# Performance work log

Measured on AMD Instinct MI355X. Metric: run time of the kernel, lower is better.

## Reference

```python
import jax, jax.numpy as jnp
import numpy as np

NUM_CLASSES = 80
POS_OVERLAP = 0.5
NEG_OVERLAP = 0.4
REG_MEAN = 0.0
REG_STD = 0.2


def setup_inputs() -> dict:
    key = jax.random.key(0)
    k1, k2, k3, k4, k5 = jax.random.split(key, 5)
    B, N, A = 8, 64, 120000
    IMG = 800.0
    # GT annotations: [x1, y1, x2, y2, class]
    xy = jax.random.uniform(k1, (B, N, 2)) * IMG
    wh = jax.random.uniform(k2, (B, N, 2)) * 256.0 + 1.0
    boxes = jnp.concatenate([xy, xy + wh], axis=-1)
    labels = jax.random.randint(k3, (B, N, 1), 0, NUM_CLASSES).astype(jnp.float32)
    annotations_batch = jnp.concatenate([boxes, labels], axis=-1)  # [B,N,5]
    # Anchors: [x1, y1, x2, y2]
    axy = jax.random.uniform(k4, (A, 2)) * IMG
    awh = jax.random.uniform(k5, (A, 2)) * 256.0 + 1.0
    anchors = jnp.concatenate([axy, axy + awh], axis=-1)  # [A,4]
    return {"annotations_batch": annotations_batch, "anchors": anchors}


def _iou(anchors, boxes):
    # anchors [A,4], boxes [N,4] -> IoU [A,N]
    area_a = (anchors[:, 2] - anchors[:, 0]) * (anchors[:, 3] - anchors[:, 1])
    area_b = (boxes[:, 2] - boxes[:, 0]) * (boxes[:, 3] - boxes[:, 1])
    lt = jnp.maximum(anchors[:, None, :2], boxes[None, :, :2])  # [A,N,2]
    rb = jnp.minimum(anchors[:, None, 2:], boxes[None, :, 2:])  # [A,N,2]
    wh = jnp.clip(rb - lt, 0.0)
    inter = wh[..., 0] * wh[..., 1]
    union = area_a[:, None] + area_b[None, :] - inter
    return inter / jnp.maximum(union, 1e-8)


def _targets_one(annotations, anchors):
    # annotations [N,5], anchors [A,4]
    boxes = annotations[:, :4]
    labels = jax.lax.stop_gradient(annotations[:, 4]).astype(jnp.int32)  # [N]
    ov = _iou(anchors, boxes)                 # [A,N]
    best = jnp.argmax(ov, axis=1)             # [A] assigned gt per anchor
    max_ov = jnp.max(ov, axis=1)              # [A]
    positive = max_ov >= POS_OVERLAP
    ignore = (max_ov > NEG_OVERLAP) & (~positive)
    anchor_states = jnp.where(positive, 1.0, jnp.where(ignore, -1.0, 0.0))
    # Classification target: one-hot of assigned class for positive anchors
    cls_target = jax.nn.one_hot(labels[best], NUM_CLASSES, dtype=anchors.dtype)
    cls_target = cls_target * positive[:, None].astype(anchors.dtype)
    gt = boxes[best]                           # [A,4]
    wa = anchors[:, 2] - anchors[:, 0]
    ha = anchors[:, 3] - anchors[:, 1]
    scale = jnp.stack([wa, ha, wa, ha], axis=1)  # [A,4]
    reg_target = ((gt - anchors) / scale - REG_MEAN) / REG_STD
    return cls_target, reg_target, anchor_states


def reference(annotations_batch, anchors):
    return jax.vmap(lambda ann: _targets_one(ann, anchors))(annotations_batch)
```

## Files before the change

### kernel.cpp

```cpp
#include <hip/hip_runtime.h>

#define NUM_CLASSES 80
#define A_NUM 120000
#define B_NUM 8
#define N_BOX 64

__global__ __launch_bounds__(256) void compute_targets_kernel(
    const float* __restrict__ annotations,
    const float4* __restrict__ anchors4,
    float* __restrict__ out)
{
#pragma clang fp contract(off)
    __shared__ float4 sbox[N_BOX];
    __shared__ int    slab[N_BOX];
    __shared__ int    scls[256];

    const int tid = threadIdx.x;
    const int b   = blockIdx.y;
    const int a0  = blockIdx.x * 256;
    const int a   = a0 + tid;

    if (tid < N_BOX) {
        const float* ann = annotations + ((size_t)b * N_BOX + tid) * 5;
        const float x0 = ann[0], y0 = ann[1], x1 = ann[2], y1 = ann[3];
        sbox[tid] = make_float4(x0, y0, x1, y1);
        slab[tid] = (int)ann[4];
    }
    __syncthreads();

    int clsidx = -1;
    if (a < A_NUM) {
        const float4 anc = anchors4[a];
        const float wa = anc.z - anc.x;
        const float ha = anc.w - anc.y;
        const float area_a = wa * ha;

        float best_iou = -1.0f;
        int   best_j   = 0;
#pragma unroll 8
        for (int j = 0; j < N_BOX; ++j) {
            const float4 bx = sbox[j];
            const float area_b = (bx.z - bx.x) * (bx.w - bx.y);
            const float ltx = fmaxf(anc.x, bx.x);
            const float lty = fmaxf(anc.y, bx.y);
            const float rbx = fminf(anc.z, bx.z);
            const float rby = fminf(anc.w, bx.w);
            const float w = fmaxf(rbx - ltx, 0.0f);
            const float h = fmaxf(rby - lty, 0.0f);
            const float inter = w * h;
            const float uni   = (area_a + area_b) - inter;
            const float iou   = inter / fmaxf(uni, 1e-8f);
            if (iou > best_iou) { best_iou = iou; best_j = j; }
        }

        const bool positive = best_iou >= 0.5f;
        const bool ignore   = (best_iou > 0.4f) && !positive;
        const float state   = positive ? 1.0f : (ignore ? -1.0f : 0.0f);

        const float4 gt = sbox[best_j];
        float4 reg;
        reg.x = ((gt.x - anc.x) / wa) / 0.2f;
        reg.y = ((gt.y - anc.y) / ha) / 0.2f;
        reg.z = ((gt.z - anc.z) / wa) / 0.2f;
        reg.w = ((gt.w - anc.w) / ha) / 0.2f;

        const size_t CLS = (size_t)B_NUM * A_NUM * NUM_CLASSES;
        const size_t REG = (size_t)B_NUM * A_NUM * 4;
        float4* regout = (float4*)(out + CLS);
        regout[(size_t)b * A_NUM + a] = reg;
        out[CLS + REG + (size_t)b * A_NUM + a] = state;

        clsidx = positive ? slab[best_j] : -1;
    }
    scls[tid] = clsidx;
    __syncthreads();

    float4* clsout = (float4*)out + ((size_t)b * A_NUM + a0) * 20;
#pragma unroll
    for (int i = 0; i < 20; ++i) {
        const int pos = i * 256 + tid;
        const int al  = pos / 20;
        const int q   = pos - al * 20;
        if (a0 + al < A_NUM) {
            const int lab = scls[al];
            const int c0  = q * 4;
            float4 v;
            v.x = (lab == c0    ) ? 1.0f : 0.0f;
            v.y = (lab == c0 + 1) ? 1.0f : 0.0f;
            v.z = (lab == c0 + 2) ? 1.0f : 0.0f;
            v.w = (lab == c0 + 3) ? 1.0f : 0.0f;
            clsout[pos] = v;
        }
    }
}

extern "C" void kernel_launch(void* const* d_in, const int* in_sizes, int n_in,
                              void* d_out, int out_size, void* d_ws, size_t ws_size,
                              hipStream_t stream) {
    const float*  annotations = (const float*)d_in[0];
    const float4* anchors     = (const float4*)d_in[1];
    float* out = (float*)d_out;

    dim3 grid((A_NUM + 255) / 256, B_NUM);
    compute_targets_kernel<<<grid, 256, 0, stream>>>(annotations, anchors, out);
}
```

Baseline: 68.55 us.

## Use per-wavefront class scatter, nontemporal stores, and precomputed box areas

Restructures the one-hot classification write so each 64-lane wavefront expands only its own anchors, which removes the block-wide second barrier. A120000 is a multiple of 64, so whole wavefronts exit early instead of using per-element bounds checks. All output stores become nontemporal to cut cache pollution on the write-bound output. GT box areas are precomputed in shared memory and the union clamp is dropped, with an occupancy hint added to launch bounds. Dropping the 1e-8 clamp could change results when the union is zero, which only happens for degenerate boxes.

```diff
diff --git a/kernel.cpp b/kernel.cpp
--- a/kernel.cpp
+++ b/kernel.cpp
@@ -5,92 +5,93 @@
 #define B_NUM 8
 #define N_BOX 64
 
-__global__ __launch_bounds__(256) void compute_targets_kernel(
+typedef float f4 __attribute__((ext_vector_type(4)));
+
+__global__ __launch_bounds__(256, 4) void compute_targets_kernel(
     const float* __restrict__ annotations,
     const float4* __restrict__ anchors4,
     float* __restrict__ out)
 {
 #pragma clang fp contract(off)
     __shared__ float4 sbox[N_BOX];
+    __shared__ float  sarea[N_BOX];
     __shared__ int    slab[N_BOX];
     __shared__ int    scls[256];
 
-    const int tid = threadIdx.x;
-    const int b   = blockIdx.y;
-    const int a0  = blockIdx.x * 256;
-    const int a   = a0 + tid;
+    const int tid  = threadIdx.x;
+    const int wv   = tid >> 6;
+    const int lane = tid & 63;
+    const int b    = blockIdx.y;
+    const int a0   = blockIdx.x * 256;
+    const int aw0  = a0 + wv * 64;
+    const int a    = a0 + tid;
 
     if (tid < N_BOX) {
         const float* ann = annotations + ((size_t)b * N_BOX + tid) * 5;
         const float x0 = ann[0], y0 = ann[1], x1 = ann[2], y1 = ann[3];
-        sbox[tid] = make_float4(x0, y0, x1, y1);
-        slab[tid] = (int)ann[4];
+        sbox[tid]  = make_float4(x0, y0, x1, y1);
+        sarea[tid] = (x1 - x0) * (y1 - y0);
+        slab[tid]  = (int)ann[4];
     }
     __syncthreads();
 
-    int clsidx = -1;
-    if (a < A_NUM) {
-        const float4 anc = anchors4[a];
-        const float wa = anc.z - anc.x;
-        const float ha = anc.w - anc.y;
-        const float area_a = wa * ha;
+    if (aw0 >= A_NUM) return;
 
-        float best_iou = -1.0f;
-        int   best_j   = 0;
+    const float4 anc = anchors4[a];
+    const float wa = anc.z - anc.x;
+    const float ha = anc.w - anc.y;
+    const float area_a = wa * ha;
+
+    float best_iou = -1.0f;
+    int   best_j   = 0;
 #pragma unroll 8
-        for (int j = 0; j < N_BOX; ++j) {
-            const float4 bx = sbox[j];
-            const float area_b = (bx.z - bx.x) * (bx.w - bx.y);
-            const float ltx = fmaxf(anc.x, bx.x);
-            const float lty = fmaxf(anc.y, bx.y);
-            const float rbx = fminf(anc.z, bx.z);
-            const float rby = fminf(anc.w, bx.w);
-            const float w = fmaxf(rbx - ltx, 0.0f);
-            const float h = fmaxf(rby - lty, 0.0f);
-            const float inter = w * h;
-            const float uni   = (area_a + area_b) - inter;
-            const float iou   = inter / fmaxf(uni, 1e-8f);
-            if (iou > best_iou) { best_iou = iou; best_j = j; }
-        }
+    for (int j = 0; j < N_BOX; ++j) {
+        const float4 bx = sbox[j];
+        const float ltx = fmaxf(anc.x, bx.x);
+        const float lty = fmaxf(anc.y, bx.y);
+        const float rbx = fminf(anc.z, bx.z);
+        const float rby = fminf(anc.w, bx.w);
+        const float w = fmaxf(rbx - ltx, 0.0f);
+        const float h = fmaxf(rby - lty, 0.0f);
+        const float inter = w * h;
+        const float uni   = (area_a + sarea[j]) - inter;
+        const float iou   = inter / uni;
+        if (iou > best_iou) { best_iou = iou; best_j = j; }
+    }
 
-        const bool positive = best_iou >= 0.5f;
-        const bool ignore   = (best_iou > 0.4f) && !positive;
-        const float state   = positive ? 1.0f : (ignore ? -1.0f : 0.0f);
+    const bool positive = best_iou >= 0.5f;
+    const bool ignore   = (best_iou > 0.4f) && !positive;
+    const float state   = positive ? 1.0f : (ignore ? -1.0f : 0.0f);
 
-        const float4 gt = sbox[best_j];
-        float4 reg;
-        reg.x = ((gt.x - anc.x) / wa) / 0.2f;
-        reg.y = ((gt.y - anc.y) / ha) / 0.2f;
-        reg.z = ((gt.z - anc.z) / wa) / 0.2f;
-        reg.w = ((gt.w - anc.w) / ha) / 0.2f;
+    const float4 gt = sbox[best_j];
+    f4 reg;
+    reg.x = ((gt.x - anc.x) / wa) / 0.2f;
+    reg.y = ((gt.y - anc.y) / ha) / 0.2f;
+    reg.z = ((gt.z - anc.z) / wa) / 0.2f;
+    reg.w = ((gt.w - anc.w) / ha) / 0.2f;
 
-        const size_t CLS = (size_t)B_NUM * A_NUM * NUM_CLASSES;
-        const size_t REG = (size_t)B_NUM * A_NUM * 4;
-        float4* regout = (float4*)(out + CLS);
-        regout[(size_t)b * A_NUM + a] = reg;
-        out[CLS + REG + (size_t)b * A_NUM + a] = state;
+    const size_t CLS = (size_t)B_NUM * A_NUM * NUM_CLASSES;
+    const size_t REG = (size_t)B_NUM * A_NUM * 4;
+    f4* regout = (f4*)(out + CLS);
+    __builtin_nontemporal_store(reg, &regout[(size_t)b * A_NUM + a]);
+    __builtin_nontemporal_store(state, &out[CLS + REG + (size_t)b * A_NUM + a]);
 
-        clsidx = positive ? slab[best_j] : -1;
-    }
-    scls[tid] = clsidx;
-    __syncthreads();
+    scls[tid] = positive ? slab[best_j] : -1;
 
-    float4* clsout = (float4*)out + ((size_t)b * A_NUM + a0) * 20;
+    f4* clsout = (f4*)out + ((size_t)b * A_NUM + aw0) * 20;
 #pragma unroll
     for (int i = 0; i < 20; ++i) {
-        const int pos = i * 256 + tid;
+        const int pos = i * 64 + lane;
         const int al  = pos / 20;
         const int q   = pos - al * 20;
-        if (a0 + al < A_NUM) {
-            const int lab = scls[al];
-            const int c0  = q * 4;
-            float4 v;
-            v.x = (lab == c0    ) ? 1.0f : 0.0f;
-            v.y = (lab == c0 + 1) ? 1.0f : 0.0f;
-            v.z = (lab == c0 + 2) ? 1.0f : 0.0f;
-            v.w = (lab == c0 + 3) ? 1.0f : 0.0f;
-            clsout[pos] = v;
-        }
+        const int lab = scls[wv * 64 + al];
+        const int c0  = q * 4;
+        f4 v;
+        v.x = (lab == c0    ) ? 1.0f : 0.0f;
+        v.y = (lab == c0 + 1) ? 1.0f : 0.0f;
+        v.z = (lab == c0 + 2) ? 1.0f : 0.0f;
+        v.w = (lab == c0 + 3) ? 1.0f : 0.0f;
+        __builtin_nontemporal_store(v, &clsout[pos]);
     }
 }
 
```

New measurement: 60.82 us, median of 2. -11.3%, faster.
